# Kernel optimization log

Hardware: AMD Instinct MI355X
Metric: run time of the kernel (lower is better)

## Reference

```python
import jax, jax.numpy as jnp
import numpy as np

B, L, H, N, DM = 16, 32768, 64, 16, 32


def setup_inputs() -> dict:
    key = jax.random.key(0)
    ks = jax.random.split(key, 16)
    inp = {}
    inp['x'] = jax.random.normal(ks[0], (B, L, H), dtype=jnp.float32)
    inp['control_parameters'] = jax.random.uniform(ks[1], (B, 2), dtype=jnp.float32)
    inp['W0'] = jax.random.normal(ks[2], (2, DM), dtype=jnp.float32) / np.sqrt(2.0)
    inp['b0'] = jnp.zeros((DM,), dtype=jnp.float32)
    inp['W1'] = jax.random.normal(ks[3], (DM, DM), dtype=jnp.float32) / np.sqrt(DM)
    inp['b1'] = jnp.zeros((DM,), dtype=jnp.float32)
    inp['W2'] = jax.random.normal(ks[4], (DM, DM), dtype=jnp.float32) / np.sqrt(DM)
    inp['b2'] = jnp.zeros((DM,), dtype=jnp.float32)
    # BlockV1 input linear
    inp['W_lin'] = jax.random.normal(ks[5], (H, H), dtype=jnp.float32) / np.sqrt(H)
    inp['b_lin'] = jnp.zeros((H,), dtype=jnp.float32)
    # DSSM / S4D parameters (S4D-Lin init)
    log_dt_min, log_dt_max = np.log(1e-3), np.log(1e-1)
    inp['log_dt'] = (log_dt_min + (log_dt_max - log_dt_min)
                     * jax.random.uniform(ks[6], (H,), dtype=jnp.float32))
    inp['A_re'] = -0.5 * jnp.ones((H, N), dtype=jnp.float32)
    inp['A_im'] = jnp.broadcast_to(np.pi * jnp.arange(N, dtype=jnp.float32), (H, N)).copy()
    inp['C_re'] = jax.random.normal(ks[7], (H, N), dtype=jnp.float32) / np.sqrt(2.0)
    inp['C_im'] = jax.random.normal(ks[8], (H, N), dtype=jnp.float32) / np.sqrt(2.0)
    inp['D'] = jax.random.normal(ks[9], (H,), dtype=jnp.float32)
    # FiLM: Linear(DM, 2*H) -> (gamma, beta)
    inp['W_film'] = jax.random.normal(ks[10], (DM, 2 * H), dtype=jnp.float32) / np.sqrt(DM)
    inp['b_film'] = jnp.zeros((2 * H,), dtype=jnp.float32)
    return inp


def _s4d_kernel(log_dt, A_re, A_im, C_re, C_im, length):
    # Diagonal SSM (S4D) convolution kernel via ZOH discretization.
    dt = jnp.exp(log_dt)[:, None]                      # [H,1]
    A = A_re + 1j * A_im                               # [H,N]
    dtA = dt * A                                       # [H,N]
    C = (C_re + 1j * C_im) * (jnp.exp(dtA) - 1.0) / A  # [H,N]
    t = jnp.arange(length, dtype=jnp.float32)          # [L]
    # Vandermonde: K[h,l] = 2 * Re( sum_n C[h,n] * exp(dtA[h,n])^l )
    vand = jnp.exp(dtA[:, :, None] * t)                # [H,N,L] complex
    return 2.0 * jnp.einsum('hn,hnl->hl', C, vand).real


def reference(x, control_parameters, W0, b0, W1, b1, W2, b2,
              W_lin, b_lin, log_dt, A_re, A_im, C_re, C_im, D,
              W_film, b_film):
    gelu = jax.nn.gelu
    # control-parameter MLP -> conditioning vector [B, DM]
    cond = gelu(control_parameters @ W0 + b0)
    cond = gelu(cond @ W1 + b1)
    cond = gelu(cond @ W2 + b2)
    # BlockV1: Linear + act
    h = gelu(x @ W_lin + b_lin)          # [B,L,H]
    u = jnp.swapaxes(h, 1, 2)            # [B,H,L]
    length = u.shape[-1]
    # S4D global convolution via FFT (linear, non-circular)
    K = _s4d_kernel(log_dt, A_re, A_im, C_re, C_im, length)   # [H,L]
    n = 2 * length
    Kf = jnp.fft.rfft(K, n=n)            # [H, n//2+1]
    uf = jnp.fft.rfft(u, n=n)            # [B,H, n//2+1]
    y = jnp.fft.irfft(uf * Kf, n=n)[..., :length] + D[:, None] * u  # [B,H,L]
    y = jnp.swapaxes(y, 1, 2)            # [B,L,H]
    # FiLM conditioning (no batch norm)
    gb = cond @ W_film + b_film          # [B, 2H]
    g, b = jnp.split(gb, 2, axis=-1)     # [B,H] each
    y = gelu(y * g[:, None, :] + b[:, None, :])
    # side-chain gate: elementwise multiply with input
    return x * y
```

## Files before the change

### kernel.cpp

```cpp
#include <hip/hip_runtime.h>
#include <hip/hip_bf16.h>
#include <math.h>

#define B_ 16
#define L_ 32768
#define H_ 64
#define N_ 16
#define DM_ 32
#define TS_ 16
#define US_ 68
#define NG_ 8

typedef __attribute__((ext_vector_type(8))) short short8;
typedef __attribute__((ext_vector_type(4))) float floatx4;
typedef __attribute__((ext_vector_type(2))) float f32x2;

__device__ __forceinline__ float fast_gelu(float v) {
    float z = fmaf(0.044715f * v, v * v, v) * 0.7978845608028654f;
#if __has_builtin(__builtin_amdgcn_exp2f) && __has_builtin(__builtin_amdgcn_rcpf)
    float e = __builtin_amdgcn_exp2f(z * 2.8853900817779268f);
    float t = 1.0f - 2.0f * __builtin_amdgcn_rcpf(e + 1.0f);
#else
    float t = tanhf(z);
#endif
    return 0.5f * v * (1.0f + t);
}

__device__ __forceinline__ unsigned short bf16_rne(float f) {
    unsigned u = __float_as_uint(f);
    return (unsigned short)((u + 0x7FFFu + ((u >> 16) & 1u)) >> 16);
}
__device__ __forceinline__ float bf16_tof(unsigned short h) {
    return __uint_as_float(((unsigned)h) << 16);
}
__device__ __forceinline__ void cvt8(const float* f, short8* hi, short8* lo) {
    union { unsigned u[4]; short8 s; } Hh, Ll;
    #pragma unroll
    for (int jp = 0; jp < 4; ++jp) {
        unsigned short h0 = bf16_rne(f[2*jp]), h1 = bf16_rne(f[2*jp+1]);
        Hh.u[jp] = (unsigned)h0 | ((unsigned)h1 << 16);
        float l0 = f[2*jp]   - bf16_tof(h0);
        float l1 = f[2*jp+1] - bf16_tof(h1);
        Ll.u[jp] = (unsigned)bf16_rne(l0) | ((unsigned)bf16_rne(l1) << 16);
    }
    *hi = Hh.s; *lo = Ll.s;
}

__device__ __forceinline__ void pk_step(f32x2& s, f32x2 w, f32x2 uv0) {
    f32x2 t;
    asm("v_pk_fma_f32 %0, %1, %2, %3 op_sel:[1,1,0] op_sel_hi:[1,0,1] neg_lo:[1,0,0]"
        : "=v"(t) : "v"(w), "v"(s), "v"(uv0));
    asm("v_pk_fma_f32 %0, %1, %0, %2 op_sel_hi:[0,1,1]"
        : "+v"(s) : "v"(w), "v"(t));
}
__device__ __forceinline__ void pk_acc(f32x2& y, f32x2 c, f32x2 s) {
    asm("v_pk_fma_f32 %0, %1, %2, %0"
        : "+v"(y) : "v"(c), "v"(s));
}

__global__ void cond_film_kernel(const float* __restrict__ cp,
    const float* __restrict__ W0, const float* __restrict__ b0,
    const float* __restrict__ W1, const float* __restrict__ b1,
    const float* __restrict__ W2, const float* __restrict__ b2,
    const float* __restrict__ Wf, const float* __restrict__ bf,
    float* __restrict__ film) {
    __shared__ float ca[B_][DM_];
    __shared__ float cb[B_][DM_];
    int tid = threadIdx.x;
    int b = tid >> 5, j = tid & 31;
    float acc = fmaf(cp[b*2+0], W0[j], fmaf(cp[b*2+1], W0[DM_+j], b0[j]));
    ca[b][j] = fast_gelu(acc);
    __syncthreads();
    acc = b1[j];
    #pragma unroll
    for (int i = 0; i < DM_; ++i) acc = fmaf(ca[b][i], W1[i*DM_+j], acc);
    cb[b][j] = fast_gelu(acc);
    __syncthreads();
    acc = b2[j];
    #pragma unroll
    for (int i = 0; i < DM_; ++i) acc = fmaf(cb[b][i], W2[i*DM_+j], acc);
    float c2 = fast_gelu(acc);
    __syncthreads();
    ca[b][j] = c2;
    __syncthreads();
    #pragma unroll
    for (int t = 0; t < 4; ++t) {
        int k = j + DM_*t;
        float a = bf[k];
        #pragma unroll
        for (int i = 0; i < DM_; ++i) a = fmaf(ca[b][i], Wf[i*2*H_+k], a);
        film[b*2*H_ + k] = a;
    }
}

__global__ void coef_kernel(const float* __restrict__ log_dt,
    const float* __restrict__ A_re, const float* __restrict__ A_im,
    const float* __restrict__ C_re, const float* __restrict__ C_im,
    float* __restrict__ coef, float Tf) {
    int g = blockIdx.x * blockDim.x + threadIdx.x;
    if (g >= H_*N_) return;
    int h = g >> 4, n = g & 15;
    float dt = expf(log_dt[h]);
    float Ar = A_re[h*N_+n], Ai = A_im[h*N_+n];
    float ar = dt*Ar, ai = dt*Ai;
    float er = expf(ar);
    float wr = er * cosf(ai), wi = er * sinf(ai);
    float eT = expf(Tf * ar);
    float aT = Tf * ai;
    float wTr = eT * cosf(aT), wTi = eT * sinf(aT);
    float d  = Ar*Ar + Ai*Ai;
    float nr = wr - 1.0f, ni = wi;
    float qr = (nr*Ar + ni*Ai) / d;
    float qi = (ni*Ar - nr*Ai) / d;
    float Cr = C_re[h*N_+n], Ci = C_im[h*N_+n];
    float cr = 2.0f * (Cr*qr - Ci*qi);
    float ci = 2.0f * (Cr*qi + Ci*qr);
    coef[(n*6+0)*H_+h] = wr;
    coef[(n*6+1)*H_+h] = wi;
    coef[(n*6+2)*H_+h] = wTr;
    coef[(n*6+3)*H_+h] = wTi;
    coef[(n*6+4)*H_+h] = cr;
    coef[(n*6+5)*H_+h] = ci;
}


__global__ void scan_agg_kernel(const float* __restrict__ states,
                                const float* __restrict__ coef,
                                float* __restrict__ agg, int Cc, int G) {
    int t = blockIdx.x * blockDim.x + threadIdx.x;
    int h = t & 63, n = (t >> 6) & 15, g = (t >> 10) & (NG_-1), b = t >> 13;
    float wTr = coef[(n*6+2)*H_+h], wTi = coef[(n*6+3)*H_+h];
    const float2* sp = (const float2*)states
        + ((size_t)(b*Cc + g*G))*N_*H_ + (size_t)n*H_ + h;
    const int stride = N_*H_;
    float car = 0.f, cai = 0.f;
    float2 buf[8];
    #pragma unroll
    for (int i = 0; i < 8; ++i) buf[i] = sp[(size_t)i*stride];
    for (int cg = 0; cg < G; cg += 8) {
        float2 nb[8];
        #pragma unroll
        for (int i = 0; i < 8; ++i)
            nb[i] = (cg + 8 + i < G) ? sp[(size_t)(cg+8+i)*stride]
                                     : make_float2(0.f, 0.f);
        #pragma unroll
        for (int i = 0; i < 8; ++i) {
            float2 v = buf[i];
            float nr2 = fmaf(wTr, car, fmaf(-wTi, cai, v.x));
            float ni2 = fmaf(wTr, cai, fmaf( wTi, car, v.y));
            car = nr2; cai = ni2;
            buf[i] = nb[i];
        }
    }
    ((float2*)agg)[t] = make_float2(car, cai);
}

__global__ void scan_group_kernel(float* __restrict__ agg,
                                  const float* __restrict__ coef, int lg2G) {
    int t = blockIdx.x * blockDim.x + threadIdx.x;
    int h = t & 63, n = (t >> 6) & 15, b = t >> 10;
    float wr = coef[(n*6+2)*H_+h], wi = coef[(n*6+3)*H_+h];
    for (int i = 0; i < lg2G; ++i) {
        float nr = wr*wr - wi*wi, ni = 2.f*wr*wi;
        wr = nr; wi = ni;
    }
    float car = 0.f, cai = 0.f;
    float2* ap = (float2*)agg + (size_t)b*NG_*1024 + (size_t)n*64 + h;
    #pragma unroll
    for (int g = 0; g < NG_; ++g) {
        float2 v = ap[(size_t)g*1024];
        ap[(size_t)g*1024] = make_float2(car, cai);
        float nr = fmaf(wr, car, fmaf(-wi, cai, v.x));
        float ni = fmaf(wr, cai, fmaf( wi, car, v.y));
        car = nr; cai = ni;
    }
}

__global__ void scan_fix_kernel(float* __restrict__ states,
                                const float* __restrict__ coef,
                                const float* __restrict__ agg, int Cc, int G) {
    int t = blockIdx.x * blockDim.x + threadIdx.x;
    int h = t & 63, n = (t >> 6) & 15, g = (t >> 10) & (NG_-1), b = t >> 13;
    float wTr = coef[(n*6+2)*H_+h], wTi = coef[(n*6+3)*H_+h];
    float2* sp = (float2*)states
        + ((size_t)(b*Cc + g*G))*N_*H_ + (size_t)n*H_ + h;
    const int stride = N_*H_;
    float2 c0 = ((const float2*)agg)[t];
    float car = c0.x, cai = c0.y;
    float2 buf[8];
    #pragma unroll
    for (int i = 0; i < 8; ++i) buf[i] = sp[(size_t)i*stride];
    for (int cg = 0; cg < G; cg += 8) {
        float2 nb[8];
        #pragma unroll
        for (int i = 0; i < 8; ++i)
            nb[i] = (cg + 8 + i < G) ? sp[(size_t)(cg+8+i)*stride]
                                     : make_float2(0.f, 0.f);
        #pragma unroll
        for (int i = 0; i < 8; ++i) {
            float2 v = buf[i];
            sp[(size_t)(cg+i)*stride] = make_float2(car, cai);
            float nr2 = fmaf(wTr, car, fmaf(-wTi, cai, v.x));
            float ni2 = fmaf(wTr, cai, fmaf( wTi, car, v.y));
            car = nr2; cai = ni2;
            buf[i] = nb[i];
        }
    }
}

template<int PHASE, int CC, bool UST>
__global__ __launch_bounds__(256, 3)
void gemm_scan_kernel(const float* __restrict__ x,
                      const float* __restrict__ W_lin, const float* __restrict__ b_lin,
                      const float* __restrict__ coef, float* __restrict__ states,
                      const float* __restrict__ D, const float* __restrict__ film,
                      float* __restrict__ out, float* __restrict__ ubuf) {
    constexpr int TT = L_/CC;
    __shared__ __align__(16) unsigned short Wf[16*64*8];
    __shared__ float uld[4][TS_*US_];
    __shared__ float xld[(PHASE==3) ? 4*TS_*US_ : 4];
    const int lane = threadIdx.x & 63;
    const int wv   = threadIdx.x >> 6;
    const int q    = blockIdx.x*4 + wv;
    const int b    = q / CC;
    const int c    = q % CC;
    const int m    = lane & 15;
    const int quad = lane >> 4;

    for (int kt = 0; kt < 2; ++kt)
        for (int nt = 0; nt < 4; ++nt) {
            float f[8];
            #pragma unroll
            for (int j = 0; j < 8; ++j)
                f[j] = W_lin[(kt*32 + quad*8 + j)*H_ + nt*16 + m];
            short8 hi, lo;
            cvt8(f, &hi, &lo);
            ((short8*)Wf)[(kt*4 + nt)*64 + lane]     = hi;
            ((short8*)Wf)[((2+kt)*4 + nt)*64 + lane] = lo;
        }

    f32x2 w2[N_], s2[N_], c2[N_];
    float g_ = 0.f, be_ = 0.f, Dh = 0.f;
    #pragma unroll
    for (int n = 0; n < N_; ++n) {
        w2[n].x = coef[(n*6+0)*H_ + lane];
        w2[n].y = coef[(n*6+1)*H_ + lane];
    }
    if (PHASE == 1) {
        #pragma unroll
        for (int n = 0; n < N_; ++n) s2[n] = (f32x2){0.f, 0.f};
    } else {
        #pragma unroll
        for (int n = 0; n < N_; ++n) {
            c2[n].x = coef[(n*6+4)*H_ + lane];
            c2[n].y = coef[(n*6+5)*H_ + lane];
            size_t idx = (((size_t)q*N_ + n)*H_ + lane)*2;
            s2[n] = *(const f32x2*)(states + idx);
        }
        g_  = film[b*2*H_ + lane];
        be_ = film[b*2*H_ + H_ + lane];
        Dh  = D[lane];
    }
    float blv[4];
    #pragma unroll
    for (int nt = 0; nt < 4; ++nt) blv[nt] = b_lin[nt*16 + m];

    const size_t base = ((size_t)b*L_ + (size_t)c*TT)*H_;
    const float* xp = x + base;
    float* op = out + base;
    float* ubp = UST ? (ubuf + base) : nullptr;
    float* myu = uld[wv];
    float* myx = (PHASE==3) ? &xld[wv*TS_*US_] : nullptr;

    for (int s = 0; s < TT/TS_; ++s) {
        const float* xs = xp + s*TS_*H_;
        short8 ah[2], al[2];
        #pragma unroll
        for (int kt = 0; kt < 2; ++kt) {
            const float* src = xs + m*H_ + kt*32 + quad*8;
            float4 v0 = *(const float4*)(src);
            float4 v1 = *(const float4*)(src + 4);
            if (PHASE == 3) {
                float* dst = &myx[m*US_ + kt*32 + quad*8];
                *(float4*)(dst)     = v0;
                *(float4*)(dst + 4) = v1;
            }
            float f[8] = {v0.x, v0.y, v0.z, v0.w, v1.x, v1.y, v1.z, v1.w};
            cvt8(f, &ah[kt], &al[kt]);
        }
        #pragma unroll
        for (int nt = 0; nt < 4; ++nt) {
            floatx4 acc = {0.f, 0.f, 0.f, 0.f};
            #pragma unroll
            for (int kt = 0; kt < 2; ++kt) {
                short8 bh = ((short8*)Wf)[(kt*4 + nt)*64 + lane];
                short8 bl = ((short8*)Wf)[((2+kt)*4 + nt)*64 + lane];
                acc = __builtin_amdgcn_mfma_f32_16x16x32_bf16(ah[kt], bh, acc, 0, 0, 0);
                acc = __builtin_amdgcn_mfma_f32_16x16x32_bf16(al[kt], bh, acc, 0, 0, 0);
                acc = __builtin_amdgcn_mfma_f32_16x16x32_bf16(ah[kt], bl, acc, 0, 0, 0);
            }
            #pragma unroll
            for (int r = 0; r < 4; ++r) {
                int row = quad*4 + r;
                float uv = fast_gelu(acc[r] + blv[nt]);
                myu[row*US_ + nt*16 + m] = uv;
            }
        }
        float uvc = myu[lane];
        float xgc = (PHASE==3) ? myx[lane] : 0.f;
        for (int l = 0; l < TS_; ++l) {
            int ln = (l+1) & (TS_-1);
            float uvn = myu[ln*US_ + lane];
            float xgn = (PHASE==3) ? myx[ln*US_ + lane] : 0.f;
            f32x2 uv0 = {uvc, 0.f};
            if (PHASE == 1) {
                if (UST) ubp[(s*TS_ + l)*H_ + lane] = uvc;
                #pragma unroll
                for (int n = 0; n < N_; ++n) pk_step(s2[n], w2[n], uv0);
            } else {
                f32x2 y2 = {0.f, 0.f};
                #pragma unroll
                for (int n = 0; n < N_; ++n) {
                    pk_step(s2[n], w2[n], uv0);
                    pk_acc(y2, c2[n], s2[n]);
                }
                float y  = fmaf(Dh, uvc, y2.x - y2.y);
                float yg = fast_gelu(fmaf(y, g_, be_));
                op[(s*TS_ + l)*H_ + lane] = xgc * yg;
            }
            uvc = uvn; xgc = xgn;
        }
    }
    if (PHASE == 1) {
        #pragma unroll
        for (int n = 0; n < N_; ++n) {
            size_t idx = (((size_t)q*N_ + n)*H_ + lane)*2;
            *(f32x2*)(states + idx) = s2[n];
        }
    }
}

template<int CC>
__global__ __launch_bounds__(256, 3)
void scan_out_kernel(const float* __restrict__ u, const float* __restrict__ x,
                     const float* __restrict__ coef, const float* __restrict__ states,
                     const float* __restrict__ D, const float* __restrict__ film,
                     float* __restrict__ out) {
    constexpr int TT = L_/CC;
    constexpr int BL = 8;
    const int lane = threadIdx.x & 63;
    const int wv   = threadIdx.x >> 6;
    const int q    = blockIdx.x*4 + wv;
    const int b    = q / CC;
    f32x2 w2[N_], s2[N_], c2[N_];
    #pragma unroll
    for (int n = 0; n < N_; ++n) {
        w2[n].x = coef[(n*6+0)*H_ + lane];
        w2[n].y = coef[(n*6+1)*H_ + lane];
        c2[n].x = coef[(n*6+4)*H_ + lane];
        c2[n].y = coef[(n*6+5)*H_ + lane];
        size_t idx = (((size_t)q*N_ + n)*H_ + lane)*2;
        s2[n] = *(const f32x2*)(states + idx);
    }
    const float g_  = film[b*2*H_ + lane];
    const float be_ = film[b*2*H_ + H_ + lane];
    const float Dh  = D[lane];
    const size_t base = ((size_t)b*L_ + (size_t)(q % CC)*TT)*H_;
    const float* up = u + base;
    const float* xp = x + base;
    float* op = out + base;

    float ub[BL], xb[BL];
    #pragma unroll
    for (int i = 0; i < BL; ++i) {
        ub[i] = up[i*H_ + lane];
        xb[i] = xp[i*H_ + lane];
    }
    for (int t0 = 0; t0 < TT; t0 += BL) {
        float nu[BL] = {}, nx[BL] = {};
        if (t0 + BL < TT) {
            #pragma unroll
            for (int i = 0; i < BL; ++i) {
                nu[i] = up[(t0+BL+i)*H_ + lane];
                nx[i] = xp[(t0+BL+i)*H_ + lane];
            }
        }
        #pragma unroll
        for (int i = 0; i < BL; ++i) {
            f32x2 uv0 = {ub[i], 0.f};
            f32x2 y2 = {0.f, 0.f};
            #pragma unroll
            for (int n = 0; n < N_; ++n) {
                pk_step(s2[n], w2[n], uv0);
                pk_acc(y2, c2[n], s2[n]);
            }
            float y  = fmaf(Dh, ub[i], y2.x - y2.y);
            float yg = fast_gelu(fmaf(y, g_, be_));
            op[(t0+i)*H_ + lane] = xb[i] * yg;
            ub[i] = nu[i]; xb[i] = nx[i];
        }
    }
}

extern "C" void kernel_launch(void* const* d_in, const int* in_sizes, int n_in,
                              void* d_out, int out_size, void* d_ws, size_t ws_size,
                              hipStream_t stream) {
    const float* x     = (const float*)d_in[0];
    const float* cp    = (const float*)d_in[1];
    const float* W0    = (const float*)d_in[2];
    const float* b0    = (const float*)d_in[3];
    const float* W1    = (const float*)d_in[4];
    const float* b1    = (const float*)d_in[5];
    const float* W2    = (const float*)d_in[6];
    const float* b2    = (const float*)d_in[7];
    const float* W_lin = (const float*)d_in[8];
    const float* b_lin = (const float*)d_in[9];
    const float* log_dt= (const float*)d_in[10];
    const float* A_re  = (const float*)d_in[11];
    const float* A_im  = (const float*)d_in[12];
    const float* C_re  = (const float*)d_in[13];
    const float* C_im  = (const float*)d_in[14];
    const float* D     = (const float*)d_in[15];
    const float* W_f   = (const float*)d_in[16];
    const float* b_f   = (const float*)d_in[17];
    float* out = (float*)d_out;

    float* film   = (float*)d_ws;
    float* coef   = film + B_*2*H_;
    float* states = coef + 6*H_*N_;

    cond_film_kernel<<<1, 512, 0, stream>>>(cp, W0, b0, W1, b1, W2, b2,
                                            W_f, b_f, film);

    const size_t head = (size_t)(B_*2*H_ + 6*H_*N_);
    const size_t st512 = (size_t)B_*512*N_*H_*2;
    const size_t aggsz = (size_t)B_*NG_*N_*H_*2;
    const size_t usz   = (size_t)B_*L_*H_;
    size_t need_u  = (head + st512 + aggsz + usz)*4;
    size_t need64  = (head + st512 + aggsz)*4;

    if (ws_size >= need_u) {
        const int Cc = 512, G = 64, lg2G = 6;
        float* agg  = states + st512;
        float* ubuf = agg + aggsz;
        coef_kernel<<<4, 256, 0, stream>>>(log_dt, A_re, A_im, C_re, C_im,
                                           coef, (float)(L_/Cc));
        gemm_scan_kernel<1,512,true><<<(B_*512)/4, 256, 0, stream>>>(
            x, W_lin, b_lin, coef, states, nullptr, nullptr, nullptr, ubuf);
        scan_agg_kernel<<<(B_*NG_*N_*H_)/256, 256, 0, stream>>>(states, coef,
                                                                agg, Cc, G);
        scan_group_kernel<<<(B_*N_*H_)/256, 256, 0, stream>>>(agg, coef, lg2G);
        scan_fix_kernel<<<(B_*NG_*N_*H_)/256, 256, 0, stream>>>(states, coef,
                                                                agg, Cc, G);
        scan_out_kernel<512><<<(B_*512)/4, 256, 0, stream>>>(
            ubuf, x, coef, states, D, film, out);
    } else if (ws_size >= need64) {
        const int Cc = 512, G = 64, lg2G = 6;
        float* agg = states + st512;
        coef_kernel<<<4, 256, 0, stream>>>(log_dt, A_re, A_im, C_re, C_im,
                                           coef, (float)(L_/Cc));
        gemm_scan_kernel<1,512,false><<<(B_*512)/4, 256, 0, stream>>>(
            x, W_lin, b_lin, coef, states, nullptr, nullptr, nullptr, nullptr);
        scan_agg_kernel<<<(B_*NG_*N_*H_)/256, 256, 0, stream>>>(states, coef,
                                                                agg, Cc, G);
        scan_group_kernel<<<(B_*N_*H_)/256, 256, 0, stream>>>(agg, coef, lg2G);
        scan_fix_kernel<<<(B_*NG_*N_*H_)/256, 256, 0, stream>>>(states, coef,
                                                                agg, Cc, G);
        gemm_scan_kernel<3,512,false><<<(B_*512)/4, 256, 0, stream>>>(
            x, W_lin, b_lin, coef, states, D, film, out, nullptr);
    } else {
        const int Cc = 256, G = 32, lg2G = 5;
        float* agg = states + (size_t)B_*256*N_*H_*2;
        coef_kernel<<<4, 256, 0, stream>>>(log_dt, A_re, A_im, C_re, C_im,
                                           coef, (float)(L_/Cc));
        gemm_scan_kernel<1,256,false><<<(B_*256)/4, 256, 0, stream>>>(
            x, W_lin, b_lin, coef, states, nullptr, nullptr, nullptr, nullptr);
        scan_agg_kernel<<<(B_*NG_*N_*H_)/256, 256, 0, stream>>>(states, coef,
                                                                agg, Cc, G);
        scan_group_kernel<<<(B_*N_*H_)/256, 256, 0, stream>>>(agg, coef, lg2G);
        scan_fix_kernel<<<(B_*NG_*N_*H_)/256, 256, 0, stream>>>(states, coef,
                                                                agg, Cc, G);
        gemm_scan_kernel<3,256,false><<<(B_*256)/4, 256, 0, stream>>>(
            x, W_lin, b_lin, coef, states, D, film, out, nullptr);
    }
}
```

Measured before the change: 440.4 us.

## Fuse three scan carry kernels into one cooperative kernel with grid sync

Replaces the separate aggregate, group-scan and fix-up kernels with one cooperative-launched kernel that computes per-group carries, does a grid-wide sync, and then rescans the chunk states with the right prefix. This removes two kernel launches and their gaps, and the group-level scan is recomputed serially per thread instead of in a separate kernel. It also peels the last block of the output loop so the prefetch branch goes away. The grid is 512 blocks of 256 threads, which must all be co-resident for the cooperative launch; if the launch fails it falls back to the old three kernels.

```diff
diff --git a/kernel.cpp b/kernel.cpp
--- a/kernel.cpp
+++ b/kernel.cpp
@@ -1,4 +1,5 @@
 #include <hip/hip_runtime.h>
+#include <hip/hip_cooperative_groups.h>
 #include <hip/hip_bf16.h>
 #include <math.h>
 
@@ -123,6 +124,78 @@
     coef[(n*6+5)*H_+h] = ci;
 }
 
+__global__ void scan_mid_kernel(float* __restrict__ states,
+                                const float* __restrict__ coef,
+                                float* __restrict__ agg,
+                                int Cc, int G, int lg2G) {
+    int t = blockIdx.x * blockDim.x + threadIdx.x;
+    int h = t & 63, n = (t >> 6) & 15, g = (t >> 10) & (NG_-1), b = t >> 13;
+    float wTr = coef[(n*6+2)*H_+h], wTi = coef[(n*6+3)*H_+h];
+    float2* sp = (float2*)states
+        + ((size_t)(b*Cc + g*G))*N_*H_ + (size_t)n*H_ + h;
+    const int stride = N_*H_;
+    float car = 0.f, cai = 0.f;
+    {
+        float2 buf[8];
+        #pragma unroll
+        for (int i = 0; i < 8; ++i) buf[i] = sp[(size_t)i*stride];
+        for (int cg = 0; cg < G; cg += 8) {
+            float2 nb[8];
+            #pragma unroll
+            for (int i = 0; i < 8; ++i)
+                nb[i] = (cg + 8 + i < G) ? sp[(size_t)(cg+8+i)*stride]
+                                         : make_float2(0.f, 0.f);
+            #pragma unroll
+            for (int i = 0; i < 8; ++i) {
+                float2 v = buf[i];
+                float nr2 = fmaf(wTr, car, fmaf(-wTi, cai, v.x));
+                float ni2 = fmaf(wTr, cai, fmaf( wTi, car, v.y));
+                car = nr2; cai = ni2;
+                buf[i] = nb[i];
+            }
+        }
+    }
+    ((float2*)agg)[t] = make_float2(car, cai);
+    __threadfence();
+    cooperative_groups::this_grid().sync();
+    __threadfence();
+    float wGr = wTr, wGi = wTi;
+    for (int i = 0; i < lg2G; ++i) {
+        float nr = wGr*wGr - wGi*wGi, ni = 2.f*wGr*wGi;
+        wGr = nr; wGi = ni;
+    }
+    float pr = 0.f, pi = 0.f;
+    const float2* ap = (const float2*)agg
+        + (size_t)b*NG_*(N_*H_) + (size_t)n*H_ + h;
+    for (int gp = 0; gp < g; ++gp) {
+        float2 v = ap[(size_t)gp*(N_*H_)];
+        float nr = fmaf(wGr, pr, fmaf(-wGi, pi, v.x));
+        float ni = fmaf(wGr, pi, fmaf( wGi, pr, v.y));
+        pr = nr; pi = ni;
+    }
+    car = pr; cai = pi;
+    {
+        float2 buf[8];
+        #pragma unroll
+        for (int i = 0; i < 8; ++i) buf[i] = sp[(size_t)i*stride];
+        for (int cg = 0; cg < G; cg += 8) {
+            float2 nb[8];
+            #pragma unroll
+            for (int i = 0; i < 8; ++i)
+                nb[i] = (cg + 8 + i < G) ? sp[(size_t)(cg+8+i)*stride]
+                                         : make_float2(0.f, 0.f);
+            #pragma unroll
+            for (int i = 0; i < 8; ++i) {
+                float2 v = buf[i];
+                sp[(size_t)(cg+i)*stride] = make_float2(car, cai);
+                float nr2 = fmaf(wTr, car, fmaf(-wTi, cai, v.x));
+                float ni2 = fmaf(wTr, cai, fmaf( wTi, car, v.y));
+                car = nr2; cai = ni2;
+                buf[i] = nb[i];
+            }
+        }
+    }
+}
 
 __global__ void scan_agg_kernel(const float* __restrict__ states,
                                 const float* __restrict__ coef,
@@ -376,14 +449,13 @@
         ub[i] = up[i*H_ + lane];
         xb[i] = xp[i*H_ + lane];
     }
-    for (int t0 = 0; t0 < TT; t0 += BL) {
-        float nu[BL] = {}, nx[BL] = {};
-        if (t0 + BL < TT) {
-            #pragma unroll
-            for (int i = 0; i < BL; ++i) {
-                nu[i] = up[(t0+BL+i)*H_ + lane];
-                nx[i] = xp[(t0+BL+i)*H_ + lane];
-            }
+    int t0 = 0;
+    for (; t0 < TT - BL; t0 += BL) {
+        float nu[BL], nx[BL];
+        #pragma unroll
+        for (int i = 0; i < BL; ++i) {
+            nu[i] = up[(t0+BL+i)*H_ + lane];
+            nx[i] = xp[(t0+BL+i)*H_ + lane];
         }
         #pragma unroll
         for (int i = 0; i < BL; ++i) {
@@ -399,6 +471,19 @@
             op[(t0+i)*H_ + lane] = xb[i] * yg;
             ub[i] = nu[i]; xb[i] = nx[i];
         }
+    }
+    #pragma unroll
+    for (int i = 0; i < BL; ++i) {
+        f32x2 uv0 = {ub[i], 0.f};
+        f32x2 y2 = {0.f, 0.f};
+        #pragma unroll
+        for (int n = 0; n < N_; ++n) {
+            pk_step(s2[n], w2[n], uv0);
+            pk_acc(y2, c2[n], s2[n]);
+        }
+        float y  = fmaf(Dh, ub[i], y2.x - y2.y);
+        float yg = fast_gelu(fmaf(y, g_, be_));
+        op[(t0+i)*H_ + lane] = xb[i] * yg;
     }
 }
 
@@ -440,18 +525,25 @@
     size_t need64  = (head + st512 + aggsz)*4;
 
     if (ws_size >= need_u) {
-        const int Cc = 512, G = 64, lg2G = 6;
+        int Cc = 512, G = 64, lg2G = 6;
         float* agg  = states + st512;
         float* ubuf = agg + aggsz;
         coef_kernel<<<4, 256, 0, stream>>>(log_dt, A_re, A_im, C_re, C_im,
                                            coef, (float)(L_/Cc));
         gemm_scan_kernel<1,512,true><<<(B_*512)/4, 256, 0, stream>>>(
             x, W_lin, b_lin, coef, states, nullptr, nullptr, nullptr, ubuf);
-        scan_agg_kernel<<<(B_*NG_*N_*H_)/256, 256, 0, stream>>>(states, coef,
-                                                                agg, Cc, G);
-        scan_group_kernel<<<(B_*N_*H_)/256, 256, 0, stream>>>(agg, coef, lg2G);
-        scan_fix_kernel<<<(B_*NG_*N_*H_)/256, 256, 0, stream>>>(states, coef,
-                                                                agg, Cc, G);
+        void* kargs[] = {(void*)&states, (void*)&coef, (void*)&agg,
+                         (void*)&Cc, (void*)&G, (void*)&lg2G};
+        hipError_t cerr = hipLaunchCooperativeKernel(
+            (const void*)scan_mid_kernel, dim3((B_*NG_*N_*H_)/256), dim3(256),
+            kargs, 0, stream);
+        if (cerr != hipSuccess) {
+            scan_agg_kernel<<<(B_*NG_*N_*H_)/256, 256, 0, stream>>>(states, coef,
+                                                                    agg, Cc, G);
+            scan_group_kernel<<<(B_*N_*H_)/256, 256, 0, stream>>>(agg, coef, lg2G);
+            scan_fix_kernel<<<(B_*NG_*N_*H_)/256, 256, 0, stream>>>(states, coef,
+                                                                    agg, Cc, G);
+        }
         scan_out_kernel<512><<<(B_*512)/4, 256, 0, stream>>>(
             ubuf, x, coef, states, D, film, out);
     } else if (ws_size >= need64) {
```

New measurement: 581.0 us. 1.32x slower.
